# Kernel optimization log

Hardware: AMD Instinct MI355X
Metric: run time of the kernel (lower is better)

Reference implementation:

```python
import jax, jax.numpy as jnp
import numpy as np

EPS = 1e-07
NEG_DIAG = -10.0
HDCE_GAMMA = 1.0

def l2_normalize(x):
    # norm = (sum(x^2, axis=1))^(1/2); out = x / (norm + 1e-7)
    norm = jnp.sqrt(jnp.sum(x * x, axis=1, keepdims=True))
    return x / (norm + EPS)

def setup_inputs() -> dict:
    key = jax.random.key(0)
    k1, k2, k3 = jax.random.split(key, 3)
    N, D, DG = 4096, 256, 256
    feat_q = jax.random.normal(k1, (N, D), dtype=jnp.float32)
    feat_k = jax.random.normal(k2, (N, D), dtype=jnp.float32)
    feat_g = jax.random.normal(k3, (N, DG), dtype=jnp.float32)
    return {"feat_q": feat_q, "feat_k": feat_k, "feat_g": feat_g}

def reference(feat_q, feat_k, feat_g):
    N = feat_q.shape[0]
    fq = l2_normalize(feat_q)  # computed in original but unused for weight_out
    fk = l2_normalize(feat_k)
    fg = l2_normalize(feat_g)
    # batched self-similarity with batch_dim_for_bmm = 1 -> [1, N, N]
    spatial_k = jnp.einsum('nd,md->nm', fk, fk)[None]
    spatial_g = jnp.einsum('nd,md->nm', fg, fg)[None]
    spatial_kg = (spatial_k + 1.0 + EPS) / (spatial_g + 1.0 + EPS)
    diag = jnp.eye(N, dtype=bool)[None]  # [1, N, N]
    weight_seed = jnp.where(diag, NEG_DIAG, spatial_kg)
    weight_out = jax.nn.softmax(weight_seed / HDCE_GAMMA, axis=2)
    wmax = jnp.max(weight_out, axis=2, keepdims=True)
    return weight_out / wmax
```

## Files before the change

kernel.cpp:

```cpp
#include <hip/hip_runtime.h>
#include <hip/hip_bf16.h>
#include <cmath>

typedef __attribute__((ext_vector_type(8))) short short8;
typedef __attribute__((ext_vector_type(4))) float f32x4;

#define EPS_F 1e-7f
#define NEG_DIAG_F -10.0f

#define BM 128
#define BN 128
#define BK 64
#define NTHREADS 512
#define PADW 132
#define NPART 32

__device__ __forceinline__ void gload_lds16(const void* gptr, void* ldsptr) {
    __builtin_amdgcn_global_load_lds(
        (const __attribute__((address_space(1))) unsigned int*)gptr,
        (__attribute__((address_space(3))) unsigned int*)ldsptr,
        16, 0, 0);
}

__global__ void norm_cast_kernel(const float* __restrict__ fk, const float* __restrict__ fg,
                                 __hip_bfloat16* __restrict__ fkb, __hip_bfloat16* __restrict__ fgb,
                                 int N, int D) {
    int n = blockIdx.x;
    int t = threadIdx.x;
    float xk = fk[(size_t)n * D + t];
    float xg = fg[(size_t)n * D + t];
    float sk = xk * xk, sg = xg * xg;
#pragma unroll
    for (int off = 32; off > 0; off >>= 1) {
        sk += __shfl_xor(sk, off, 64);
        sg += __shfl_xor(sg, off, 64);
    }
    __shared__ float lsk[4], lsg[4];
    int w = t >> 6, l = t & 63;
    if (l == 0) { lsk[w] = sk; lsg[w] = sg; }
    __syncthreads();
    sk = lsk[0] + lsk[1] + lsk[2] + lsk[3];
    sg = lsg[0] + lsg[1] + lsg[2] + lsg[3];
    float rkv = 1.0f / (sqrtf(sk) + EPS_F);
    float rgv = 1.0f / (sqrtf(sg) + EPS_F);
    fkb[(size_t)n * D + t] = __float2bfloat16(xk * rkv);
    fgb[(size_t)n * D + t] = __float2bfloat16(xg * rgv);
}

__global__ __launch_bounds__(NTHREADS) void dual_gram_kernel(
    const __hip_bfloat16* __restrict__ fkb, const __hip_bfloat16* __restrict__ fgb,
    float* __restrict__ out, float* __restrict__ P, int N, int D) {

    __shared__ __align__(16) char smem[PADW * 128 * 4 + 1024];
    float* bounce = (float*)smem;
    int* lmax = (int*)(smem + PADW * 128 * 4);

    int bx = blockIdx.x, by = blockIdx.y;
    if (by > bx) return;
    int r0 = by * BM, c0 = bx * BN;

    int t = threadIdx.x;
    int w = t >> 6, l = t & 63;
    int wr = w >> 2, wc = w & 3;
    int lr = l & 15, lg = l >> 4;

    char* lAk = smem;
    char* lBk = smem + 16384;
    char* lAg = smem + 32768;
    char* lBg = smem + 49152;

    f32x4 acck[4][2], accg[4][2];
    f32x4 zero = {0.f, 0.f, 0.f, 0.f};
#pragma unroll
    for (int m = 0; m < 4; ++m)
#pragma unroll
        for (int n = 0; n < 2; ++n) { acck[m][n] = zero; accg[m][n] = zero; }

    const size_t rowbytes = (size_t)D * 2;

    for (int k0 = 0; k0 < D; k0 += BK) {
#pragma unroll
        for (int c = 0; c < 2; ++c) {
            int o = (t + c * NTHREADS) * 16;
            int row = o >> 7;
            int csw = (o & 127) ^ ((row & 7) << 4);
            size_t goffA = (size_t)(r0 + row) * rowbytes + (size_t)k0 * 2 + csw;
            size_t goffB = (size_t)(c0 + row) * rowbytes + (size_t)k0 * 2 + csw;
            int ldsoff = (w << 10) + (c << 13);
            gload_lds16((const char*)fkb + goffA, lAk + ldsoff);
            gload_lds16((const char*)fkb + goffB, lBk + ldsoff);
            gload_lds16((const char*)fgb + goffA, lAg + ldsoff);
            gload_lds16((const char*)fgb + goffB, lBg + ldsoff);
        }
        __syncthreads();

#pragma unroll
        for (int kk = 0; kk < BK; kk += 32) {
            int kb = (kk + lg * 8) * 2;
            short8 ak[4], ag[4], bk2[2], bg2[2];
#pragma unroll
            for (int m = 0; m < 4; ++m) {
                int row = wr * 64 + m * 16 + lr;
                int o = (row << 7) + kb;
                o ^= ((row & 7) << 4);
                ak[m] = *(const short8*)(lAk + o);
                ag[m] = *(const short8*)(lAg + o);
            }
#pragma unroll
            for (int n = 0; n < 2; ++n) {
                int row = wc * 32 + n * 16 + lr;
                int o = (row << 7) + kb;
                o ^= ((row & 7) << 4);
                bk2[n] = *(const short8*)(lBk + o);
                bg2[n] = *(const short8*)(lBg + o);
            }
#pragma unroll
            for (int m = 0; m < 4; ++m)
#pragma unroll
                for (int n = 0; n < 2; ++n) {
                    acck[m][n] = __builtin_amdgcn_mfma_f32_16x16x32_bf16(ak[m], bk2[n], acck[m][n], 0, 0, 0);
                    accg[m][n] = __builtin_amdgcn_mfma_f32_16x16x32_bf16(ag[m], bg2[n], accg[m][n], 0, 0, 0);
                }
        }
        __syncthreads();
    }

    if (t < 256) lmax[t] = 0;

    int lcol[2];
#pragma unroll
    for (int n = 0; n < 2; ++n) lcol[n] = wc * 32 + n * 16 + lr;

#pragma unroll
    for (int m = 0; m < 4; ++m)
#pragma unroll
        for (int j = 0; j < 4; ++j) {
            int lrow = wr * 64 + m * 16 + lg * 4 + j;
#pragma unroll
            for (int n = 0; n < 2; ++n) {
                float dk = acck[m][n][j];
                float dg = accg[m][n][j];
                float s = (dk + 1.0f + EPS_F) * __builtin_amdgcn_rcpf(dg + 1.0f + EPS_F);
                if (r0 + lrow == c0 + lcol[n]) s = NEG_DIAG_F;
                acck[m][n][j] = s;
            }
        }
    __syncthreads();

#pragma unroll
    for (int m = 0; m < 4; ++m)
#pragma unroll
        for (int j = 0; j < 4; ++j) {
            float pm = fmaxf(acck[m][0][j], acck[m][1][j]);
#pragma unroll
            for (int off = 1; off < 16; off <<= 1)
                pm = fmaxf(pm, __shfl_xor(pm, off, 64));
            if (lr == 0) atomicMax(&lmax[wr * 64 + m * 16 + lg * 4 + j], __float_as_int(pm));
        }
#pragma unroll
    for (int n = 0; n < 2; ++n) {
        float cm = acck[0][n][0];
#pragma unroll
        for (int m = 0; m < 4; ++m)
#pragma unroll
            for (int j = 0; j < 4; ++j) cm = fmaxf(cm, acck[m][n][j]);
        cm = fmaxf(cm, __shfl_xor(cm, 16, 64));
        cm = fmaxf(cm, __shfl_xor(cm, 32, 64));
        if (l < 16) atomicMax(&lmax[128 + lcol[n]], __float_as_int(cm));
    }

#pragma unroll
    for (int m = 0; m < 4; ++m)
#pragma unroll
        for (int n = 0; n < 2; ++n)
#pragma unroll
            for (int j = 0; j < 4; ++j)
                bounce[(wr * 64 + m * 16 + lg * 4 + j) * PADW + lcol[n]] = acck[m][n][j];
    __syncthreads();

#pragma unroll
    for (int i = 0; i < 8; ++i) {
        int r = (t >> 5) + 16 * i;
        int k = t & 31;
        f32x4 v = *(const f32x4*)(bounce + r * PADW + 4 * k);
        *(f32x4*)(out + (size_t)(r0 + r) * N + c0 + 4 * k) = v;
    }
    if (t < 128) {
        P[(size_t)(r0 + t) * NPART + bx] = __int_as_float(lmax[t]);
    } else if (t < 256 && by != bx) {
        P[(size_t)(c0 + t - 128) * NPART + by] = __int_as_float(lmax[t]);
    }

    if (by != bx) {
        __syncthreads();
#pragma unroll
        for (int m = 0; m < 4; ++m)
#pragma unroll
            for (int n = 0; n < 2; ++n)
#pragma unroll
                for (int j = 0; j < 4; ++j)
                    bounce[lcol[n] * PADW + (wr * 64 + m * 16 + lg * 4 + j)] = acck[m][n][j];
        __syncthreads();
#pragma unroll
        for (int i = 0; i < 8; ++i) {
            int cc = (t >> 5) + 16 * i;
            int k = t & 31;
            f32x4 v = *(const f32x4*)(bounce + cc * PADW + 4 * k);
            *(f32x4*)(out + (size_t)(c0 + cc) * N + r0 + 4 * k) = v;
        }
    }
}

__global__ void finalize_kernel(float* __restrict__ out, const float* __restrict__ P, int N) {
    int row = blockIdx.x;
    int t = threadIdx.x;
    float m = P[(size_t)row * NPART + (t & 31)];
#pragma unroll
    for (int off = 1; off < 32; off <<= 1)
        m = fmaxf(m, __shfl_xor(m, off, 64));
    float4* o4 = (float4*)(out + (size_t)row * N);
    int n4 = N >> 2;
    for (int i = t; i < n4; i += 256) {
        float4 v = o4[i];
        v.x = __expf(v.x - m);
        v.y = __expf(v.y - m);
        v.z = __expf(v.z - m);
        v.w = __expf(v.w - m);
        o4[i] = v;
    }
}

extern "C" void kernel_launch(void* const* d_in, const int* in_sizes, int n_in,
                              void* d_out, int out_size, void* d_ws, size_t ws_size,
                              hipStream_t stream) {
    const float* fk = (const float*)d_in[1];
    const float* fg = (const float*)d_in[2];
    float* out = (float*)d_out;

    int N = (int)llround(sqrt((double)out_size));
    int D = in_sizes[1] / N;

    char* ws = (char*)d_ws;
    float* P = (float*)ws;
    __hip_bfloat16* fkb = (__hip_bfloat16*)(ws + (size_t)N * NPART * 4);
    __hip_bfloat16* fgb = (__hip_bfloat16*)(ws + (size_t)N * NPART * 4 + (size_t)N * D * 2);

    norm_cast_kernel<<<N, D, 0, stream>>>(fk, fg, fkb, fgb, N, D);

    int nt = N / BN;
    dual_gram_kernel<<<dim3(nt, nt), NTHREADS, 0, stream>>>(fkb, fgb, out, P, N, D);

    finalize_kernel<<<N, 256, 0, stream>>>(out, P, N);
}
```

Baseline: 65.60 us.

## Use 128x64 symmetric tiles with shuffle transpose and direct global stores

Tiles change from 128x128 with 512 threads to 128x64 with 256 threads, and the triangular tile selection is adjusted to match. The LDS bounce buffer used for the output transpose is removed: each 4x4 fragment is transposed in registers with cross-lane shuffles and written straight to global memory in both the normal and mirrored orientation. This cuts LDS use and barriers, which should allow more blocks per CU. In exchange the global stores are narrower and less coalesced. The partial-max buffer grows to 96 slots, is zeroed in the norm kernel, and the MFMA loop is wrapped in s_setprio.

```diff
diff --git a/kernel.cpp b/kernel.cpp
--- a/kernel.cpp
+++ b/kernel.cpp
@@ -9,11 +9,10 @@
 #define NEG_DIAG_F -10.0f
 
 #define BM 128
-#define BN 128
+#define BN 64
 #define BK 64
-#define NTHREADS 512
-#define PADW 132
-#define NPART 32
+#define NTHREADS 256
+#define NPART 96
 
 __device__ __forceinline__ void gload_lds16(const void* gptr, void* ldsptr) {
     __builtin_amdgcn_global_load_lds(
@@ -22,9 +21,22 @@
         16, 0, 0);
 }
 
+__device__ __forceinline__ f32x4 xpose4(f32x4 v, int q) {
+    f32x4 tt, wv, t2, xv;
+    tt[0] = __shfl_xor(v[0], 1, 64); tt[1] = __shfl_xor(v[1], 1, 64);
+    tt[2] = __shfl_xor(v[2], 1, 64); tt[3] = __shfl_xor(v[3], 1, 64);
+    if (q & 1) { wv[0] = tt[1]; wv[1] = v[1]; wv[2] = tt[3]; wv[3] = v[3]; }
+    else       { wv[0] = v[0];  wv[1] = tt[0]; wv[2] = v[2]; wv[3] = tt[2]; }
+    t2[0] = __shfl_xor(wv[0], 2, 64); t2[1] = __shfl_xor(wv[1], 2, 64);
+    t2[2] = __shfl_xor(wv[2], 2, 64); t2[3] = __shfl_xor(wv[3], 2, 64);
+    if (q & 2) { xv[0] = t2[2]; xv[1] = t2[3]; xv[2] = wv[2]; xv[3] = wv[3]; }
+    else       { xv[0] = wv[0]; xv[1] = wv[1]; xv[2] = t2[0]; xv[3] = t2[1]; }
+    return xv;
+}
+
 __global__ void norm_cast_kernel(const float* __restrict__ fk, const float* __restrict__ fg,
                                  __hip_bfloat16* __restrict__ fkb, __hip_bfloat16* __restrict__ fgb,
-                                 int N, int D) {
+                                 float* __restrict__ P, int N, int D) {
     int n = blockIdx.x;
     int t = threadIdx.x;
     float xk = fk[(size_t)n * D + t];
@@ -45,29 +57,29 @@
     float rgv = 1.0f / (sqrtf(sg) + EPS_F);
     fkb[(size_t)n * D + t] = __float2bfloat16(xk * rkv);
     fgb[(size_t)n * D + t] = __float2bfloat16(xg * rgv);
+    if (t < NPART) P[(size_t)n * NPART + t] = 0.0f;
 }
 
 __global__ __launch_bounds__(NTHREADS) void dual_gram_kernel(
     const __hip_bfloat16* __restrict__ fkb, const __hip_bfloat16* __restrict__ fgb,
     float* __restrict__ out, float* __restrict__ P, int N, int D) {
 
-    __shared__ __align__(16) char smem[PADW * 128 * 4 + 1024];
-    float* bounce = (float*)smem;
-    int* lmax = (int*)(smem + PADW * 128 * 4);
+    __shared__ __align__(16) char smem[49152 + 768];
+    int* lmax = (int*)(smem + 49152);
 
     int bx = blockIdx.x, by = blockIdx.y;
-    if (by > bx) return;
+    if (bx < 2 * by) return;
     int r0 = by * BM, c0 = bx * BN;
 
     int t = threadIdx.x;
     int w = t >> 6, l = t & 63;
-    int wr = w >> 2, wc = w & 3;
+    int wr = w >> 1, wc = w & 1;
     int lr = l & 15, lg = l >> 4;
 
     char* lAk = smem;
-    char* lBk = smem + 16384;
-    char* lAg = smem + 32768;
-    char* lBg = smem + 49152;
+    char* lAg = smem + 16384;
+    char* lBk = smem + 32768;
+    char* lBg = smem + 40960;
 
     f32x4 acck[4][2], accg[4][2];
     f32x4 zero = {0.f, 0.f, 0.f, 0.f};
@@ -79,18 +91,25 @@
     const size_t rowbytes = (size_t)D * 2;
 
     for (int k0 = 0; k0 < D; k0 += BK) {
+#pragma unroll
+        for (int c = 0; c < 4; ++c) {
+            int o = (t + c * NTHREADS) * 16;
+            int row = o >> 7;
+            int csw = (o & 127) ^ ((row & 7) << 4);
+            size_t goff = (size_t)(r0 + row) * rowbytes + (size_t)k0 * 2 + csw;
+            int dst = (w << 10) + (c << 12);
+            gload_lds16((const char*)fkb + goff, lAk + dst);
+            gload_lds16((const char*)fgb + goff, lAg + dst);
+        }
 #pragma unroll
         for (int c = 0; c < 2; ++c) {
             int o = (t + c * NTHREADS) * 16;
             int row = o >> 7;
             int csw = (o & 127) ^ ((row & 7) << 4);
-            size_t goffA = (size_t)(r0 + row) * rowbytes + (size_t)k0 * 2 + csw;
-            size_t goffB = (size_t)(c0 + row) * rowbytes + (size_t)k0 * 2 + csw;
-            int ldsoff = (w << 10) + (c << 13);
-            gload_lds16((const char*)fkb + goffA, lAk + ldsoff);
-            gload_lds16((const char*)fkb + goffB, lBk + ldsoff);
-            gload_lds16((const char*)fgb + goffA, lAg + ldsoff);
-            gload_lds16((const char*)fgb + goffB, lBg + ldsoff);
+            size_t goff = (size_t)(c0 + row) * rowbytes + (size_t)k0 * 2 + csw;
+            int dst = (w << 10) + (c << 12);
+            gload_lds16((const char*)fkb + goff, lBk + dst);
+            gload_lds16((const char*)fgb + goff, lBg + dst);
         }
         __syncthreads();
 
@@ -114,6 +133,7 @@
                 bk2[n] = *(const short8*)(lBk + o);
                 bg2[n] = *(const short8*)(lBg + o);
             }
+            __builtin_amdgcn_s_setprio(1);
 #pragma unroll
             for (int m = 0; m < 4; ++m)
 #pragma unroll
@@ -121,11 +141,12 @@
                     acck[m][n] = __builtin_amdgcn_mfma_f32_16x16x32_bf16(ak[m], bk2[n], acck[m][n], 0, 0, 0);
                     accg[m][n] = __builtin_amdgcn_mfma_f32_16x16x32_bf16(ag[m], bg2[n], accg[m][n], 0, 0, 0);
                 }
+            __builtin_amdgcn_s_setprio(0);
         }
         __syncthreads();
     }
 
-    if (t < 256) lmax[t] = 0;
+    if (t < 192) lmax[t] = 0;
 
     int lcol[2];
 #pragma unroll
@@ -166,55 +187,39 @@
             for (int j = 0; j < 4; ++j) cm = fmaxf(cm, acck[m][n][j]);
         cm = fmaxf(cm, __shfl_xor(cm, 16, 64));
         cm = fmaxf(cm, __shfl_xor(cm, 32, 64));
-        if (l < 16) atomicMax(&lmax[128 + lcol[n]], __float_as_int(cm));
-    }
-
-#pragma unroll
-    for (int m = 0; m < 4; ++m)
-#pragma unroll
-        for (int n = 0; n < 2; ++n)
-#pragma unroll
-            for (int j = 0; j < 4; ++j)
-                bounce[(wr * 64 + m * 16 + lg * 4 + j) * PADW + lcol[n]] = acck[m][n][j];
+        if (lg == 0) atomicMax(&lmax[128 + lcol[n]], __float_as_int(cm));
+    }
+
+    int q = lr & 3;
+#pragma unroll
+    for (int m = 0; m < 4; ++m)
+#pragma unroll
+        for (int n = 0; n < 2; ++n) {
+            f32x4 v = acck[m][n];
+            f32x4 xv = xpose4(v, q);
+            int drow = r0 + wr * 64 + m * 16 + lg * 4 + q;
+            int dcol = c0 + wc * 32 + n * 16 + (lr >> 2) * 4;
+            *(f32x4*)(out + (size_t)drow * N + dcol) = xv;
+            int trow = c0 + lcol[n];
+            int tcol = r0 + wr * 64 + m * 16 + lg * 4;
+            *(f32x4*)(out + (size_t)trow * N + tcol) = v;
+        }
+
     __syncthreads();
-
-#pragma unroll
-    for (int i = 0; i < 8; ++i) {
-        int r = (t >> 5) + 16 * i;
-        int k = t & 31;
-        f32x4 v = *(const f32x4*)(bounce + r * PADW + 4 * k);
-        *(f32x4*)(out + (size_t)(r0 + r) * N + c0 + 4 * k) = v;
-    }
     if (t < 128) {
         P[(size_t)(r0 + t) * NPART + bx] = __int_as_float(lmax[t]);
-    } else if (t < 256 && by != bx) {
-        P[(size_t)(c0 + t - 128) * NPART + by] = __int_as_float(lmax[t]);
-    }
-
-    if (by != bx) {
-        __syncthreads();
-#pragma unroll
-        for (int m = 0; m < 4; ++m)
-#pragma unroll
-            for (int n = 0; n < 2; ++n)
-#pragma unroll
-                for (int j = 0; j < 4; ++j)
-                    bounce[lcol[n] * PADW + (wr * 64 + m * 16 + lg * 4 + j)] = acck[m][n][j];
-        __syncthreads();
-#pragma unroll
-        for (int i = 0; i < 8; ++i) {
-            int cc = (t >> 5) + 16 * i;
-            int k = t & 31;
-            f32x4 v = *(const f32x4*)(bounce + cc * PADW + 4 * k);
-            *(f32x4*)(out + (size_t)(c0 + cc) * N + r0 + 4 * k) = v;
-        }
+    } else if (t < 192) {
+        P[(size_t)(c0 + t - 128) * NPART + 64 + by] = __int_as_float(lmax[t]);
     }
 }
 
 __global__ void finalize_kernel(float* __restrict__ out, const float* __restrict__ P, int N) {
     int row = blockIdx.x;
     int t = threadIdx.x;
-    float m = P[(size_t)row * NPART + (t & 31)];
+    int j = t & 31;
+    float m = P[(size_t)row * NPART + j];
+    m = fmaxf(m, P[(size_t)row * NPART + 32 + j]);
+    m = fmaxf(m, P[(size_t)row * NPART + 64 + j]);
 #pragma unroll
     for (int off = 1; off < 32; off <<= 1)
         m = fmaxf(m, __shfl_xor(m, off, 64));
@@ -245,10 +250,9 @@
     __hip_bfloat16* fkb = (__hip_bfloat16*)(ws + (size_t)N * NPART * 4);
     __hip_bfloat16* fgb = (__hip_bfloat16*)(ws + (size_t)N * NPART * 4 + (size_t)N * D * 2);
 
-    norm_cast_kernel<<<N, D, 0, stream>>>(fk, fg, fkb, fgb, N, D);
-
-    int nt = N / BN;
-    dual_gram_kernel<<<dim3(nt, nt), NTHREADS, 0, stream>>>(fkb, fgb, out, P, N, D);
+    norm_cast_kernel<<<N, D, 0, stream>>>(fk, fg, fkb, fgb, P, N, D);
+
+    dual_gram_kernel<<<dim3(N / BN, N / BM), NTHREADS, 0, stream>>>(fkb, fgb, out, P, N, D);
 
     finalize_kernel<<<N, 256, 0, stream>>>(out, P, N);
 }
```

After: 74.62 us. 1.14x slower.

## Replace LDS-staged 128x128 dual Gram tiles with single-wave 64x32 register-fed tiles

Applied to the files above, without the earlier changes.

Replaces the 512-thread LDS-staged block GEMM with one-wave blocks that load bf16 MFMA operands straight from global memory into registers over the full K=256. Each block computes a 64x32 tile of both Gram matrices and writes the tile and its mirror through a small LDS bounce. Per-tile row and column maxima go directly into a widened partial-max buffer, which norm_cast zeroes, and finalize reduces that buffer. This aims to remove LDS staging and barriers and to raise occupancy and grid parallelism, at the cost of losing operand reuse across waves, so global and L2 traffic for operands goes up.

```diff
diff --git a/kernel.cpp b/kernel.cpp
--- a/kernel.cpp
+++ b/kernel.cpp
@@ -7,24 +7,11 @@
 
 #define EPS_F 1e-7f
 #define NEG_DIAG_F -10.0f
-
-#define BM 128
-#define BN 128
-#define BK 64
-#define NTHREADS 512
-#define PADW 132
-#define NPART 32
-
-__device__ __forceinline__ void gload_lds16(const void* gptr, void* ldsptr) {
-    __builtin_amdgcn_global_load_lds(
-        (const __attribute__((address_space(1))) unsigned int*)gptr,
-        (__attribute__((address_space(3))) unsigned int*)ldsptr,
-        16, 0, 0);
-}
+#define NPART 192
 
 __global__ void norm_cast_kernel(const float* __restrict__ fk, const float* __restrict__ fg,
                                  __hip_bfloat16* __restrict__ fkb, __hip_bfloat16* __restrict__ fgb,
-                                 int N, int D) {
+                                 float* __restrict__ P, int N, int D) {
     int n = blockIdx.x;
     int t = threadIdx.x;
     float xk = fk[(size_t)n * D + t];
@@ -45,29 +32,21 @@
     float rgv = 1.0f / (sqrtf(sg) + EPS_F);
     fkb[(size_t)n * D + t] = __float2bfloat16(xk * rkv);
     fgb[(size_t)n * D + t] = __float2bfloat16(xg * rgv);
-}
-
-__global__ __launch_bounds__(NTHREADS) void dual_gram_kernel(
+    if (t < NPART) P[(size_t)n * NPART + t] = 0.0f;
+}
+
+__global__ __launch_bounds__(64) void gram_wave_kernel(
     const __hip_bfloat16* __restrict__ fkb, const __hip_bfloat16* __restrict__ fgb,
     float* __restrict__ out, float* __restrict__ P, int N, int D) {
 
-    __shared__ __align__(16) char smem[PADW * 128 * 4 + 1024];
-    float* bounce = (float*)smem;
-    int* lmax = (int*)(smem + PADW * 128 * 4);
-
     int bx = blockIdx.x, by = blockIdx.y;
-    if (by > bx) return;
-    int r0 = by * BM, c0 = bx * BN;
-
-    int t = threadIdx.x;
-    int w = t >> 6, l = t & 63;
-    int wr = w >> 2, wc = w & 3;
+    if (bx < 2 * by) return;
+    int r0 = by * 64, c0 = bx * 32;
+
+    int l = threadIdx.x;
     int lr = l & 15, lg = l >> 4;
 
-    char* lAk = smem;
-    char* lBk = smem + 16384;
-    char* lAg = smem + 32768;
-    char* lBg = smem + 49152;
+    __shared__ __align__(16) float bnc[64 * 36];
 
     f32x4 acck[4][2], accg[4][2];
     f32x4 zero = {0.f, 0.f, 0.f, 0.f};
@@ -76,76 +55,50 @@
 #pragma unroll
         for (int n = 0; n < 2; ++n) { acck[m][n] = zero; accg[m][n] = zero; }
 
-    const size_t rowbytes = (size_t)D * 2;
-
-    for (int k0 = 0; k0 < D; k0 += BK) {
-#pragma unroll
-        for (int c = 0; c < 2; ++c) {
-            int o = (t + c * NTHREADS) * 16;
-            int row = o >> 7;
-            int csw = (o & 127) ^ ((row & 7) << 4);
-            size_t goffA = (size_t)(r0 + row) * rowbytes + (size_t)k0 * 2 + csw;
-            size_t goffB = (size_t)(c0 + row) * rowbytes + (size_t)k0 * 2 + csw;
-            int ldsoff = (w << 10) + (c << 13);
-            gload_lds16((const char*)fkb + goffA, lAk + ldsoff);
-            gload_lds16((const char*)fkb + goffB, lBk + ldsoff);
-            gload_lds16((const char*)fgb + goffA, lAg + ldsoff);
-            gload_lds16((const char*)fgb + goffB, lBg + ldsoff);
-        }
-        __syncthreads();
-
-#pragma unroll
-        for (int kk = 0; kk < BK; kk += 32) {
-            int kb = (kk + lg * 8) * 2;
-            short8 ak[4], ag[4], bk2[2], bg2[2];
-#pragma unroll
-            for (int m = 0; m < 4; ++m) {
-                int row = wr * 64 + m * 16 + lr;
-                int o = (row << 7) + kb;
-                o ^= ((row & 7) << 4);
-                ak[m] = *(const short8*)(lAk + o);
-                ag[m] = *(const short8*)(lAg + o);
+    const __hip_bfloat16* bAk = fkb + (size_t)(r0 + lr) * D + lg * 8;
+    const __hip_bfloat16* bAg = fgb + (size_t)(r0 + lr) * D + lg * 8;
+    const __hip_bfloat16* bBk = fkb + (size_t)(c0 + lr) * D + lg * 8;
+    const __hip_bfloat16* bBg = fgb + (size_t)(c0 + lr) * D + lg * 8;
+    size_t rstep = (size_t)16 * D;
+
+#pragma unroll
+    for (int kk = 0; kk < 8; ++kk) {
+        short8 ak[4], ag[4], bk[2], bg[2];
+#pragma unroll
+        for (int m = 0; m < 4; ++m) {
+            ak[m] = *(const short8*)(bAk + (size_t)m * rstep + kk * 32);
+            ag[m] = *(const short8*)(bAg + (size_t)m * rstep + kk * 32);
+        }
+#pragma unroll
+        for (int n = 0; n < 2; ++n) {
+            bk[n] = *(const short8*)(bBk + (size_t)n * rstep + kk * 32);
+            bg[n] = *(const short8*)(bBg + (size_t)n * rstep + kk * 32);
+        }
+        __builtin_amdgcn_s_setprio(1);
+#pragma unroll
+        for (int m = 0; m < 4; ++m)
+#pragma unroll
+            for (int n = 0; n < 2; ++n) {
+                acck[m][n] = __builtin_amdgcn_mfma_f32_16x16x32_bf16(ak[m], bk[n], acck[m][n], 0, 0, 0);
+                accg[m][n] = __builtin_amdgcn_mfma_f32_16x16x32_bf16(ag[m], bg[n], accg[m][n], 0, 0, 0);
             }
-#pragma unroll
-            for (int n = 0; n < 2; ++n) {
-                int row = wc * 32 + n * 16 + lr;
-                int o = (row << 7) + kb;
-                o ^= ((row & 7) << 4);
-                bk2[n] = *(const short8*)(lBk + o);
-                bg2[n] = *(const short8*)(lBg + o);
-            }
-#pragma unroll
-            for (int m = 0; m < 4; ++m)
-#pragma unroll
-                for (int n = 0; n < 2; ++n) {
-                    acck[m][n] = __builtin_amdgcn_mfma_f32_16x16x32_bf16(ak[m], bk2[n], acck[m][n], 0, 0, 0);
-                    accg[m][n] = __builtin_amdgcn_mfma_f32_16x16x32_bf16(ag[m], bg2[n], accg[m][n], 0, 0, 0);
-                }
-        }
-        __syncthreads();
-    }
-
-    if (t < 256) lmax[t] = 0;
-
-    int lcol[2];
-#pragma unroll
-    for (int n = 0; n < 2; ++n) lcol[n] = wc * 32 + n * 16 + lr;
+        __builtin_amdgcn_s_setprio(0);
+    }
 
 #pragma unroll
     for (int m = 0; m < 4; ++m)
 #pragma unroll
         for (int j = 0; j < 4; ++j) {
-            int lrow = wr * 64 + m * 16 + lg * 4 + j;
+            int lrow = m * 16 + lg * 4 + j;
 #pragma unroll
             for (int n = 0; n < 2; ++n) {
                 float dk = acck[m][n][j];
                 float dg = accg[m][n][j];
                 float s = (dk + 1.0f + EPS_F) * __builtin_amdgcn_rcpf(dg + 1.0f + EPS_F);
-                if (r0 + lrow == c0 + lcol[n]) s = NEG_DIAG_F;
+                if (r0 + lrow == c0 + n * 16 + lr) s = NEG_DIAG_F;
                 acck[m][n][j] = s;
             }
         }
-    __syncthreads();
 
 #pragma unroll
     for (int m = 0; m < 4; ++m)
@@ -155,58 +108,56 @@
 #pragma unroll
             for (int off = 1; off < 16; off <<= 1)
                 pm = fmaxf(pm, __shfl_xor(pm, off, 64));
-            if (lr == 0) atomicMax(&lmax[wr * 64 + m * 16 + lg * 4 + j], __float_as_int(pm));
-        }
-#pragma unroll
-    for (int n = 0; n < 2; ++n) {
-        float cm = acck[0][n][0];
+            if (lr == 0)
+                P[(size_t)(r0 + m * 16 + lg * 4 + j) * NPART + bx] = pm;
+        }
+
+    bool doT = (bx > 2 * by + 1);
+    if (doT) {
+#pragma unroll
+        for (int n = 0; n < 2; ++n) {
+            float cm = acck[0][n][0];
+#pragma unroll
+            for (int m = 0; m < 4; ++m)
+#pragma unroll
+                for (int j = 0; j < 4; ++j) cm = fmaxf(cm, acck[m][n][j]);
+            cm = fmaxf(cm, __shfl_xor(cm, 16, 64));
+            cm = fmaxf(cm, __shfl_xor(cm, 32, 64));
+            if (lg == 0)
+                P[(size_t)(c0 + n * 16 + lr) * NPART + 128 + by] = cm;
+        }
+    }
+
+#pragma unroll
+    for (int m = 0; m < 4; ++m)
+#pragma unroll
+        for (int n = 0; n < 2; ++n)
+#pragma unroll
+            for (int j = 0; j < 4; ++j)
+                bnc[(m * 16 + lg * 4 + j) * 36 + n * 16 + lr] = acck[m][n][j];
+    __syncthreads();
+#pragma unroll
+    for (int i = 0; i < 8; ++i) {
+        int rr = i * 8 + (l >> 3);
+        f32x4 v = *(const f32x4*)&bnc[rr * 36 + (l & 7) * 4];
+        *(f32x4*)(out + (size_t)(r0 + rr) * N + c0 + (l & 7) * 4) = v;
+    }
+
+    if (doT) {
+        __syncthreads();
 #pragma unroll
         for (int m = 0; m < 4; ++m)
 #pragma unroll
-            for (int j = 0; j < 4; ++j) cm = fmaxf(cm, acck[m][n][j]);
-        cm = fmaxf(cm, __shfl_xor(cm, 16, 64));
-        cm = fmaxf(cm, __shfl_xor(cm, 32, 64));
-        if (l < 16) atomicMax(&lmax[128 + lcol[n]], __float_as_int(cm));
-    }
-
-#pragma unroll
-    for (int m = 0; m < 4; ++m)
-#pragma unroll
-        for (int n = 0; n < 2; ++n)
-#pragma unroll
-            for (int j = 0; j < 4; ++j)
-                bounce[(wr * 64 + m * 16 + lg * 4 + j) * PADW + lcol[n]] = acck[m][n][j];
-    __syncthreads();
-
-#pragma unroll
-    for (int i = 0; i < 8; ++i) {
-        int r = (t >> 5) + 16 * i;
-        int k = t & 31;
-        f32x4 v = *(const f32x4*)(bounce + r * PADW + 4 * k);
-        *(f32x4*)(out + (size_t)(r0 + r) * N + c0 + 4 * k) = v;
-    }
-    if (t < 128) {
-        P[(size_t)(r0 + t) * NPART + bx] = __int_as_float(lmax[t]);
-    } else if (t < 256 && by != bx) {
-        P[(size_t)(c0 + t - 128) * NPART + by] = __int_as_float(lmax[t]);
-    }
-
-    if (by != bx) {
+            for (int n = 0; n < 2; ++n)
+#pragma unroll
+                for (int j = 0; j < 4; ++j)
+                    bnc[(n * 16 + lr) * 68 + m * 16 + lg * 4 + j] = acck[m][n][j];
         __syncthreads();
 #pragma unroll
-        for (int m = 0; m < 4; ++m)
-#pragma unroll
-            for (int n = 0; n < 2; ++n)
-#pragma unroll
-                for (int j = 0; j < 4; ++j)
-                    bounce[lcol[n] * PADW + (wr * 64 + m * 16 + lg * 4 + j)] = acck[m][n][j];
-        __syncthreads();
-#pragma unroll
         for (int i = 0; i < 8; ++i) {
-            int cc = (t >> 5) + 16 * i;
-            int k = t & 31;
-            f32x4 v = *(const f32x4*)(bounce + cc * PADW + 4 * k);
-            *(f32x4*)(out + (size_t)(c0 + cc) * N + r0 + 4 * k) = v;
+            int tr = i * 4 + (l >> 4);
+            f32x4 v = *(const f32x4*)&bnc[tr * 68 + (l & 15) * 4];
+            *(f32x4*)(out + (size_t)(c0 + tr) * N + r0 + (l & 15) * 4) = v;
         }
     }
 }
@@ -214,9 +165,12 @@
 __global__ void finalize_kernel(float* __restrict__ out, const float* __restrict__ P, int N) {
     int row = blockIdx.x;
     int t = threadIdx.x;
-    float m = P[(size_t)row * NPART + (t & 31)];
-#pragma unroll
-    for (int off = 1; off < 32; off <<= 1)
+    int j = t & 63;
+    float m = P[(size_t)row * NPART + j];
+    m = fmaxf(m, P[(size_t)row * NPART + 64 + j]);
+    m = fmaxf(m, P[(size_t)row * NPART + 128 + j]);
+#pragma unroll
+    for (int off = 1; off < 64; off <<= 1)
         m = fmaxf(m, __shfl_xor(m, off, 64));
     float4* o4 = (float4*)(out + (size_t)row * N);
     int n4 = N >> 2;
@@ -245,10 +199,9 @@
     __hip_bfloat16* fkb = (__hip_bfloat16*)(ws + (size_t)N * NPART * 4);
     __hip_bfloat16* fgb = (__hip_bfloat16*)(ws + (size_t)N * NPART * 4 + (size_t)N * D * 2);
 
-    norm_cast_kernel<<<N, D, 0, stream>>>(fk, fg, fkb, fgb, N, D);
-
-    int nt = N / BN;
-    dual_gram_kernel<<<dim3(nt, nt), NTHREADS, 0, stream>>>(fkb, fgb, out, P, N, D);
+    norm_cast_kernel<<<N, D, 0, stream>>>(fk, fg, fkb, fgb, P, N, D);
+
+    gram_wave_kernel<<<dim3(N / 32, N / 64), 64, 0, stream>>>(fkb, fgb, out, P, N, D);
 
     finalize_kernel<<<N, 256, 0, stream>>>(out, P, N);
 }
```

Result: slower. 110.8 us (+69.0%).
